# Performance work log

Measured on AMD Instinct MI355X. Metric: run time of the kernel, lower is better.

Reference implementation:

```python
import jax, jax.numpy as jnp
import numpy as np

B, D, N, MH, MV = 4, 1024, 2048, 1024, 1024

def setup_inputs() -> dict:
    key = jax.random.key(0)
    k1, k2, k3, k4, k5 = jax.random.split(key, 5)
    return {
        "x": jax.random.normal(k1, (B, D, N), dtype=jnp.float32),
        "W_Q": jax.random.normal(k2, (MH, D), dtype=jnp.float32),
        "W_K": jax.random.normal(k3, (MH, D), dtype=jnp.float32),
        "W_V": jax.random.normal(k4, (MV, D), dtype=jnp.float32),
        "W_O": jax.random.normal(k5, (D, MV), dtype=jnp.float32),
    }

def reference(x, W_Q, W_K, W_V, W_O):
    # x: [b, d, n] (feature-major). Projections: [b, m, n]
    q = jnp.einsum('hd,bdn->bhn', W_Q, x)
    k = jnp.einsum('hd,bdn->bhn', W_K, x)
    v = jnp.einsum('vd,bdn->bvn', W_V, x)
    # scores[b,i,j] = sum_h k[b,h,i] * q[b,h,j]  -> [b, n, n]; NOTE: no 1/sqrt scale (faithful)
    scores = jnp.einsum('bhi,bhj->bij', k, q)
    scores = jax.nn.softmax(scores, axis=-1)
    # v @ scores -> [b, m_V, n]
    attn = jnp.einsum('bvi,bij->bvj', v, scores)
    # W_O @ attn -> [b, d, n]
    return jnp.einsum('dv,bvj->bdj', W_O, attn)
```

## Files before the change

### kernel.cpp

```cpp
#include <hip/hip_runtime.h>
#include <cstddef>
#include <cstdint>

typedef unsigned short u16;
typedef __attribute__((ext_vector_type(8))) short bf16x8;
typedef __attribute__((ext_vector_type(8))) _Float16 f16x8;
typedef __attribute__((ext_vector_type(4))) float f32x4;
typedef __attribute__((ext_vector_type(16))) float f32x16;

#define GLOBAL_AS __attribute__((address_space(1)))
#define LDS_AS __attribute__((address_space(3)))

__device__ __forceinline__ void async16(const u16* g, u16* l) {
    __builtin_amdgcn_global_load_lds((GLOBAL_AS const uint32_t*)g,
                                     (LDS_AS uint32_t*)l, 16, 0, 0);
}

__device__ __forceinline__ u16 f2bf(float f) {
    uint32_t u = __builtin_bit_cast(uint32_t, f);
    uint32_t r = (u + 0x7FFFu + ((u >> 16) & 1u)) >> 16;
    return (u16)r;
}

__global__ __launch_bounds__(256)
void wcast(const float4* __restrict__ src, u16* __restrict__ dst)
{
    int i = blockIdx.x * 256 + threadIdx.x;
    float4 v = src[i];
    ushort4 a = { f2bf(v.x), f2bf(v.y), f2bf(v.z), f2bf(v.w) };
    *(ushort4*)&dst[4 * (size_t)i] = a;
}

__global__ __launch_bounds__(256)
void tsplit_h2(const float* __restrict__ Sb, size_t sBatch,
               u16* __restrict__ Db, size_t dBatch, size_t plane,
               int R, int C)
{
    const float* S = Sb + blockIdx.z * sBatch;
    u16* D = Db + blockIdx.z * dBatch;
    __shared__ float t[32][33];
    int tx = threadIdx.x & 31, ty = threadIdx.x >> 5;
    int c0 = blockIdx.x * 32, r0 = blockIdx.y * 32;
    #pragma unroll
    for (int k = 0; k < 4; ++k)
        t[ty + 8 * k][tx] = S[(size_t)(r0 + ty + 8 * k) * C + c0 + tx];
    __syncthreads();
    #pragma unroll
    for (int k = 0; k < 4; ++k) {
        float a = t[tx][ty + 8 * k] * 64.0f;
        _Float16 h0 = (_Float16)a;
        _Float16 h1 = (_Float16)(a - (float)h0);
        size_t o = (size_t)(c0 + ty + 8 * k) * R + r0 + tx;
        D[o] = __builtin_bit_cast(u16, h0);
        D[plane + o] = __builtin_bit_cast(u16, h1);
    }
}

__global__ __launch_bounds__(256)
void xprep(const float* __restrict__ Sb, size_t sBatch,
           u16* __restrict__ BFb, size_t bfBatch,
           u16* __restrict__ Db, size_t dBatch, size_t plane)
{
    const float* S = Sb + blockIdx.z * sBatch;
    u16* BF = BFb + blockIdx.z * bfBatch;
    u16* D = Db + blockIdx.z * dBatch;
    __shared__ float t[32][33];
    int tx = threadIdx.x & 31, ty = threadIdx.x >> 5;
    int c0 = blockIdx.x * 32, r0 = blockIdx.y * 32;
    #pragma unroll
    for (int k = 0; k < 4; ++k) {
        float v = S[(size_t)(r0 + ty + 8 * k) * 2048 + c0 + tx];
        t[ty + 8 * k][tx] = v;
        BF[(size_t)(r0 + ty + 8 * k) * 2048 + c0 + tx] = f2bf(v);
    }
    __syncthreads();
    #pragma unroll
    for (int k = 0; k < 4; ++k) {
        float a = t[tx][ty + 8 * k] * 64.0f;
        _Float16 h0 = (_Float16)a;
        _Float16 h1 = (_Float16)(a - (float)h0);
        size_t o = (size_t)(c0 + ty + 8 * k) * 1024 + r0 + tx;
        D[o] = __builtin_bit_cast(u16, h0);
        D[plane + o] = __builtin_bit_cast(u16, h1);
    }
}

__global__ __launch_bounds__(256)
void tcast(const float* __restrict__ S, u16* __restrict__ D, int R, int C)
{
    __shared__ float t[32][33];
    int tx = threadIdx.x & 31, ty = threadIdx.x >> 5;
    int c0 = blockIdx.x * 32, r0 = blockIdx.y * 32;
    #pragma unroll
    for (int k = 0; k < 4; ++k)
        t[ty + 8 * k][tx] = S[(size_t)(r0 + ty + 8 * k) * C + c0 + tx];
    __syncthreads();
    #pragma unroll
    for (int k = 0; k < 4; ++k)
        D[(size_t)(c0 + ty + 8 * k) * R + r0 + tx] = f2bf(t[tx][ty + 8 * k]);
}

__global__ __launch_bounds__(256)
void tbf16(const u16* __restrict__ Sb, size_t sBatch, u16* __restrict__ Db, size_t dBatch)
{
    const u16* S = Sb + blockIdx.z * sBatch;
    u16* D = Db + blockIdx.z * dBatch;
    __shared__ u16 t[32][34];
    int tx = threadIdx.x & 31, ty = threadIdx.x >> 5;
    int c0 = blockIdx.x * 32, r0 = blockIdx.y * 32;
    #pragma unroll
    for (int k = 0; k < 4; ++k)
        t[ty + 8 * k][tx] = S[(size_t)(r0 + ty + 8 * k) * 2048 + c0 + tx];
    __syncthreads();
    #pragma unroll
    for (int k = 0; k < 4; ++k)
        D[(size_t)(c0 + ty + 8 * k) * 2048 + r0 + tx] = t[tx][ty + 8 * k];
}

#define MMF4(AF, BF)                                                                   \
    _Pragma("unroll") for (int i = 0; i < 4; ++i)                                      \
        _Pragma("unroll") for (int j = 0; j < 4; ++j)                                  \
            acc[i][j] = __builtin_amdgcn_mfma_f32_16x16x32_f16(AF[i], BF[j], acc[i][j], 0, 0, 0);
#define MMB4(AF, BF)                                                                   \
    _Pragma("unroll") for (int i = 0; i < 4; ++i)                                      \
        _Pragma("unroll") for (int j = 0; j < 4; ++j)                                  \
            acc[i][j] = __builtin_amdgcn_mfma_f32_16x16x32_bf16(AF[i], BF[j], acc[i][j], 0, 0, 0);

template<int TERMS, int EPI>
__global__ __launch_bounds__(256)
void gemm_big(const u16* __restrict__ Ab, size_t aBatch, size_t aPlane,
              const u16* __restrict__ Bb, size_t bBatch, size_t bPlane,
              void* __restrict__ Cb, size_t cBatch, size_t cPlane,
              int M, int N, int K)
{
    constexpr int RSZ = 4096;
    constexpr int BUF = (TERMS == 3 ? 4 : 2) * RSZ;
    __shared__ u16 lds[2 * BUF];
    const u16* A = Ab + blockIdx.z * aBatch;
    const u16* B = Bb + blockIdx.z * bBatch;
    const int tid = threadIdx.x;
    const int lane = tid & 63, wave = tid >> 6;
    const int m0 = blockIdx.y * 128, n0 = blockIdx.x * 128;
    const int l15 = lane & 15, q = lane >> 4;
    const int rm = (wave >> 1) * 64, rn = (wave & 1) * 64;

    int sr[2], sg[2], sbase[2];
    #pragma unroll
    for (int it = 0; it < 2; ++it) {
        int s = tid + it * 256;
        sr[it] = s >> 2;
        sg[it] = (s & 3) ^ ((sr[it] >> 1) & 3);
        sbase[it] = (it * 256 + wave * 64) * 8;
    }
    const int fsw = (q ^ ((l15 >> 1) & 3)) * 8;
    int aoff[4], boff[4];
    #pragma unroll
    for (int f = 0; f < 4; ++f) {
        aoff[f] = (rm + f * 16 + l15) * 32 + fsw;
        boff[f] = (rn + f * 16 + l15) * 32 + fsw;
    }

    f32x4 acc[4][4];
    #pragma unroll
    for (int i = 0; i < 4; ++i)
        #pragma unroll
        for (int j = 0; j < 4; ++j)
            acc[i][j] = (f32x4){0.f, 0.f, 0.f, 0.f};

#define STAGEB(PP, KT)                                                                 \
    do {                                                                               \
        _Pragma("unroll")                                                              \
        for (int it = 0; it < 2; ++it) {                                               \
            const size_t ao = (size_t)(m0 + sr[it]) * K + (KT) + sg[it] * 8;           \
            const size_t bo = (size_t)(n0 + sr[it]) * K + (KT) + sg[it] * 8;           \
            const int d = (PP) * BUF + sbase[it];                                      \
            if (TERMS == 3) {                                                          \
                async16(A + ao, &lds[d]);                                              \
                async16(A + aPlane + ao, &lds[d + RSZ]);                               \
                async16(B + bo, &lds[d + 2 * RSZ]);                                    \
                async16(B + bPlane + bo, &lds[d + 3 * RSZ]);                           \
            } else {                                                                   \
                async16(A + ao, &lds[d]);                                              \
                async16(B + bo, &lds[d + RSZ]);                                        \
            }                                                                          \
        }                                                                              \
    } while (0)

    STAGEB(0, 0);
    for (int kt = 0; kt < K; kt += 32) {
        const int p = (kt >> 5) & 1;
        __syncthreads();
        if (kt + 32 < K) STAGEB(p ^ 1, kt + 32);
        const u16* L = &lds[p * BUF];
        if (TERMS == 3) {
            f16x8 a0f[4], b0f[4], xf[4];
            #pragma unroll
            for (int f = 0; f < 4; ++f) a0f[f] = *(const f16x8*)&L[aoff[f]];
            #pragma unroll
            for (int f = 0; f < 4; ++f) b0f[f] = *(const f16x8*)&L[2 * RSZ + boff[f]];
            MMF4(a0f, b0f);
            #pragma unroll
            for (int f = 0; f < 4; ++f) xf[f] = *(const f16x8*)&L[3 * RSZ + boff[f]];
            MMF4(a0f, xf);
            #pragma unroll
            for (int f = 0; f < 4; ++f) xf[f] = *(const f16x8*)&L[RSZ + aoff[f]];
            MMF4(xf, b0f);
        } else {
            bf16x8 af[4], bf_[4];
            #pragma unroll
            for (int f = 0; f < 4; ++f) af[f] = *(const bf16x8*)&L[aoff[f]];
            #pragma unroll
            for (int f = 0; f < 4; ++f) bf_[f] = *(const bf16x8*)&L[RSZ + boff[f]];
            MMB4(af, bf_);
        }
    }
#undef STAGEB

    #pragma unroll
    for (int i = 0; i < 4; ++i) {
        int row = m0 + rm + i * 16 + q * 4;
        #pragma unroll
        for (int j = 0; j < 4; ++j) {
            int col = n0 + rn + j * 16 + l15;
            #pragma unroll
            for (int r = 0; r < 4; ++r) {
                float v = acc[i][j][r];
                size_t o = (size_t)(row + r) * N + col;
                if (EPI == 0) {
                    ((float*)Cb + blockIdx.z * cBatch)[o] = v;
                } else if (EPI == 1) {
                    u16* C0 = (u16*)Cb + blockIdx.z * cBatch;
                    float vs = v * 0.000244140625f;
                    _Float16 h0 = (_Float16)vs;
                    _Float16 h1 = (_Float16)(vs - (float)h0);
                    C0[o] = __builtin_bit_cast(u16, h0);
                    C0[cPlane + o] = __builtin_bit_cast(u16, h1);
                } else {
                    ((u16*)Cb + blockIdx.z * cBatch)[o] = f2bf(v);
                }
            }
        }
    }
}

template<int TERMS, int EPI, int TM, int TN, int WGM, int WGN>
__global__ __launch_bounds__(512, 2)
void gemm_w(const u16* __restrict__ Ab, size_t aBatch, size_t aPlane,
            const u16* __restrict__ Bb, size_t bBatch, size_t bPlane,
            void* __restrict__ Cb, size_t cBatch, size_t cPlane,
            int M, int N, int K)
{
    constexpr int ASZ = TM * 32;
    constexpr int BSZ = TN * 32;
    constexpr int APL = (TERMS == 3) ? 2 : 1;
    constexpr int BUF = APL * (ASZ + BSZ);
    constexpr int FM = TM / WGM / 32;
    constexpr int FN = TN / WGN / 32;
    constexpr int AIT = TM / 128;
    constexpr int BIT = TN / 128;
    extern __shared__ __align__(16) u16 lds[];

    int bid = blockIdx.x + gridDim.x * blockIdx.y;
    int cpr = gridDim.x >> 2;
    int c8 = bid & 7, kk = bid >> 3;
    int bx = (kk % cpr) * 4 + (c8 & 3);
    int by = (kk / cpr) * 2 + (c8 >> 2);

    const u16* A = Ab + blockIdx.z * aBatch;
    const u16* B = Bb + blockIdx.z * bBatch;
    const int tid = threadIdx.x;
    const int lane = tid & 63, wave = tid >> 6;
    const int m0 = by * TM, n0 = bx * TN;
    const int l31 = lane & 31, half = lane >> 5;
    const int rm = (wave / WGN) * (TM / WGM);
    const int rn = (wave % WGN) * (TN / WGN);

    int arow[FM], asw[FM], brow[FN], bsw[FN];
    #pragma unroll
    for (int f = 0; f < FM; ++f) { arow[f] = rm + f * 32 + l31; asw[f] = (arow[f] >> 1) & 3; }
    #pragma unroll
    for (int f = 0; f < FN; ++f) { brow[f] = rn + f * 32 + l31; bsw[f] = (brow[f] >> 1) & 3; }

    f32x16 acc[FM][FN];
    #pragma unroll
    for (int i = 0; i < FM; ++i)
        #pragma unroll
        for (int j = 0; j < FN; ++j)
            #pragma unroll
            for (int r = 0; r < 16; ++r) acc[i][j][r] = 0.f;

    auto stage = [&](int pp, int kt) {
        #pragma unroll
        for (int it = 0; it < AIT; ++it) {
            int s = tid + it * 512;
            int r = s >> 2;
            int g = (s & 3) ^ ((r >> 1) & 3);
            int base = pp * BUF + (it * 512 + wave * 64) * 8;
            size_t go = (size_t)(m0 + r) * K + kt + g * 8;
            async16(A + go, &lds[base]);
            if (TERMS == 3) async16(A + aPlane + go, &lds[base + ASZ]);
        }
        #pragma unroll
        for (int it = 0; it < BIT; ++it) {
            int s = tid + it * 512;
            int r = s >> 2;
            int g = (s & 3) ^ ((r >> 1) & 3);
            int base = pp * BUF + APL * ASZ + (it * 512 + wave * 64) * 8;
            size_t go = (size_t)(n0 + r) * K + kt + g * 8;
            async16(B + go, &lds[base]);
            if (TERMS == 3) async16(B + bPlane + go, &lds[base + BSZ]);
        }
    };

#define RDAF(dst, PL, H)                                                               \
    _Pragma("unroll")                                                                  \
    for (int f = 0; f < FM; ++f)                                                       \
        dst[f] = *(const f16x8*)&L[(PL) * ASZ + arow[f] * 32 + ((2 * (H) + half) ^ asw[f]) * 8];
#define RDBF(dst, PL, H)                                                               \
    _Pragma("unroll")                                                                  \
    for (int f = 0; f < FN; ++f)                                                       \
        dst[f] = *(const f16x8*)&L[2 * ASZ + (PL) * BSZ + brow[f] * 32 + ((2 * (H) + half) ^ bsw[f]) * 8];
#define MMW(AF, BF)                                                                    \
    _Pragma("unroll")                                                                  \
    for (int i = 0; i < FM; ++i)                                                       \
        _Pragma("unroll")                                                              \
        for (int j = 0; j < FN; ++j)                                                   \
            acc[i][j] = __builtin_amdgcn_mfma_f32_32x32x16_f16(AF[i], BF[j], acc[i][j], 0, 0, 0);
#define MMWB(AF, BF)                                                                   \
    _Pragma("unroll")                                                                  \
    for (int i = 0; i < FM; ++i)                                                       \
        _Pragma("unroll")                                                              \
        for (int j = 0; j < FN; ++j)                                                   \
            acc[i][j] = __builtin_amdgcn_mfma_f32_32x32x16_bf16(AF[i], BF[j], acc[i][j], 0, 0, 0);

    stage(0, 0);
    for (int kt = 0; kt < K; kt += 32) {
        const int p = (kt >> 5) & 1;
        __syncthreads();
        if (kt + 32 < K) stage(p ^ 1, kt + 32);
        const u16* L = &lds[p * BUF];
        if (TERMS == 3) {
            f16x8 A0h0[FM], A0h1[FM], B0h0[FN], B0h1[FN];
            f16x8 B1h0[FN], B1h1[FN], A1h0[FM], A1h1[FM];
            RDAF(A0h0, 0, 0) RDBF(B0h0, 0, 0)
            RDAF(A0h1, 0, 1) RDBF(B0h1, 0, 1)
            RDBF(B1h0, 1, 0)
            MMW(A0h0, B0h0)
            RDBF(B1h1, 1, 1)
            MMW(A0h1, B0h1)
            RDAF(A1h0, 1, 0)
            MMW(A0h0, B1h0)
            MMW(A0h1, B1h1)
            RDAF(A1h1, 1, 1)
            MMW(A1h0, B0h0)
            MMW(A1h1, B0h1)
        } else {
            bf16x8 Ah0[FM], Ah1[FM], Bh0[FN], Bh1[FN];
            #pragma unroll
            for (int f = 0; f < FM; ++f)
                Ah0[f] = *(const bf16x8*)&L[arow[f] * 32 + (half ^ asw[f]) * 8];
            #pragma unroll
            for (int f = 0; f < FN; ++f)
                Bh0[f] = *(const bf16x8*)&L[ASZ + brow[f] * 32 + (half ^ bsw[f]) * 8];
            #pragma unroll
            for (int f = 0; f < FM; ++f)
                Ah1[f] = *(const bf16x8*)&L[arow[f] * 32 + ((2 + half) ^ asw[f]) * 8];
            #pragma unroll
            for (int f = 0; f < FN; ++f)
                Bh1[f] = *(const bf16x8*)&L[ASZ + brow[f] * 32 + ((2 + half) ^ bsw[f]) * 8];
            MMWB(Ah0, Bh0)
            MMWB(Ah1, Bh1)
        }
    }
#undef RDAF
#undef RDBF
#undef MMW
#undef MMWB

    #pragma unroll
    for (int i = 0; i < FM; ++i) {
        #pragma unroll
        for (int j = 0; j < FN; ++j) {
            int col = n0 + rn + j * 32 + l31;
            #pragma unroll
            for (int r = 0; r < 16; ++r) {
                int row = m0 + rm + i * 32 + (r & 3) + 8 * (r >> 2) + 4 * half;
                float v = acc[i][j][r];
                size_t o = (size_t)row * N + col;
                if (EPI == 0) {
                    ((float*)Cb + blockIdx.z * cBatch)[o] = v;
                } else if (EPI == 1) {
                    u16* C0 = (u16*)Cb + blockIdx.z * cBatch;
                    float vs = v * 0.000244140625f;
                    _Float16 h0 = (_Float16)vs;
                    _Float16 h1 = (_Float16)(vs - (float)h0);
                    C0[o] = __builtin_bit_cast(u16, h0);
                    C0[cPlane + o] = __builtin_bit_cast(u16, h1);
                } else {
                    ((u16*)Cb + blockIdx.z * cBatch)[o] = f2bf(v);
                }
            }
        }
    }
}

__global__ __launch_bounds__(256)
void softmax_p(const float* __restrict__ Sb, size_t sBatch, u16* __restrict__ Pb, size_t pBatch)
{
    const float* S = Sb + blockIdx.y * sBatch + (size_t)blockIdx.x * 2048;
    u16* P = Pb + blockIdx.y * pBatch + (size_t)blockIdx.x * 2048;
    const int tid = threadIdx.x;

    float4 v0 = *(const float4*)&S[tid * 4];
    float4 v1 = *(const float4*)&S[1024 + tid * 4];

    float m = fmaxf(fmaxf(fmaxf(v0.x, v0.y), fmaxf(v0.z, v0.w)),
                    fmaxf(fmaxf(v1.x, v1.y), fmaxf(v1.z, v1.w)));
    #pragma unroll
    for (int off = 32; off > 0; off >>= 1)
        m = fmaxf(m, __shfl_xor(m, off, 64));
    __shared__ float redm[4];
    if ((tid & 63) == 0) redm[tid >> 6] = m;
    __syncthreads();
    m = fmaxf(fmaxf(redm[0], redm[1]), fmaxf(redm[2], redm[3]));

    v0.x = __expf(v0.x - m); v0.y = __expf(v0.y - m);
    v0.z = __expf(v0.z - m); v0.w = __expf(v0.w - m);
    v1.x = __expf(v1.x - m); v1.y = __expf(v1.y - m);
    v1.z = __expf(v1.z - m); v1.w = __expf(v1.w - m);

    float s = v0.x + v0.y + v0.z + v0.w + v1.x + v1.y + v1.z + v1.w;
    #pragma unroll
    for (int off = 32; off > 0; off >>= 1)
        s += __shfl_xor(s, off, 64);
    __shared__ float reds[4];
    if ((tid & 63) == 0) reds[tid >> 6] = s;
    __syncthreads();
    s = reds[0] + reds[1] + reds[2] + reds[3];

    const float r = 1.0f / s;
    ushort4 o0 = { f2bf(v0.x * r), f2bf(v0.y * r), f2bf(v0.z * r), f2bf(v0.w * r) };
    ushort4 o1 = { f2bf(v1.x * r), f2bf(v1.y * r), f2bf(v1.z * r), f2bf(v1.w * r) };
    *(ushort4*)&P[tid * 4] = o0;
    *(ushort4*)&P[1024 + tid * 4] = o1;
}

extern "C" void kernel_launch(void* const* d_in, const int* in_sizes, int n_in,
                              void* d_out, int out_size, void* d_ws, size_t ws_size,
                              hipStream_t stream)
{
    const size_t MB = 1048576;
    const size_t WREG = 34 * MB;
    const size_t PER  = 32 * MB;
    const size_t PER_US = PER / 2, PER_F = PER / 4;

    char* ws = (char*)d_ws;
    u16* WQT2 = (u16*)ws;
    u16* WKT2 = (u16*)(ws + 4 * MB);
    u16* M2   = (u16*)(ws + 8 * MB);
    u16* WObf = (u16*)(ws + 12 * MB);
    u16* WVT  = (u16*)(ws + 14 * MB);
    u16* WOV  = (u16*)(ws + 16 * MB);
    u16* xbf  = (u16*)(ws + 18 * MB);

    int G = (ws_size >= WREG + 4 * PER) ? 4 : (ws_size >= WREG + 2 * PER) ? 2 : 1;

    const float* x = (const float*)d_in[0];
    float* out = (float*)d_out;
    dim3 blk(256);

    hipFuncSetAttribute((const void*)gemm_w<3, 0, 256, 256, 2, 4>,
                        hipFuncAttributeMaxDynamicSharedMemorySize, 131072);
    hipFuncSetAttribute((const void*)gemm_w<3, 1, 256, 128, 4, 2>,
                        hipFuncAttributeMaxDynamicSharedMemorySize, 98304);

    tsplit_h2<<<dim3(32, 32, 1), blk, 0, stream>>>((const float*)d_in[1], 0, WQT2, 0, 1048576, 1024, 1024);
    tsplit_h2<<<dim3(32, 32, 1), blk, 0, stream>>>((const float*)d_in[2], 0, WKT2, 0, 1048576, 1024, 1024);
    gemm_big<3, 1><<<dim3(8, 8, 1), blk, 0, stream>>>(WKT2, 0, 1048576, WQT2, 0, 1048576,
                                                      M2, 0, 1048576, 1024, 1024, 1024);
    wcast<<<1024, blk, 0, stream>>>((const float4*)d_in[4], WObf);
    tcast<<<dim3(32, 32, 1), blk, 0, stream>>>((const float*)d_in[3], WVT, 1024, 1024);
    gemm_big<1, 2><<<dim3(8, 8, 1), blk, 0, stream>>>(WObf, 0, 0, WVT, 0, 0,
                                                      WOV, 0, 0, 1024, 1024, 1024);

    for (int b0 = 0; b0 < 4; b0 += G) {
        char* R = ws + WREG;
        u16*   xT2 = (u16*)R;
        u16*   TT2 = (u16*)(R + 8 * MB);
        float* S32 = (float*)(R + 16 * MB);
        u16*   Pb  = (u16*)R;
        u16*   PTb = (u16*)(R + 8 * MB);
        u16*   XPT = (u16*)(R + 16 * MB);

        xprep<<<dim3(64, 32, G), blk, 0, stream>>>(x + (size_t)b0 * 2097152, 2097152,
                                                   xbf + (size_t)b0 * 2097152, 2097152,
                                                   xT2, PER_US, 2097152);
        gemm_w<3, 1, 256, 128, 4, 2><<<dim3(8, 8, G), 512, 98304, stream>>>(
            xT2, PER_US, 2097152, M2, 0, 1048576, TT2, PER_US, 2097152, 2048, 1024, 1024);
        gemm_w<3, 0, 256, 256, 2, 4><<<dim3(8, 8, G), 512, 131072, stream>>>(
            xT2, PER_US, 2097152, TT2, PER_US, 2097152, S32, PER_F, 0, 2048, 2048, 1024);
        softmax_p<<<dim3(2048, G), blk, 0, stream>>>(S32, PER_F, Pb, PER_US);
        tbf16<<<dim3(64, 64, G), blk, 0, stream>>>(Pb, PER_US, PTb, PER_US);
        gemm_w<1, 2, 256, 128, 4, 2><<<dim3(8, 8, G), 512, 49152, stream>>>(
            PTb, PER_US, 0, xbf + (size_t)b0 * 2097152, 2097152, 0,
            XPT, PER_US, 0, 2048, 1024, 2048);
        gemm_w<1, 0, 256, 128, 4, 2><<<dim3(16, 4, G), 512, 49152, stream>>>(
            WOV, 0, 0, XPT, PER_US, 0, out + (size_t)b0 * 2097152, 2097152, 0,
            1024, 2048, 1024);
    }
}
```

Before: 412.3 us.

## Fuse weight prep kernels and split-K the weight-product GEMMs with reduction

Merges the four weight-conversion kernels into one launch, using a role index in the z grid dimension. The two 1024^3 weight-product GEMMs (W_K^T W_Q and W_O W_V) previously launched only 64 blocks each; they now split K four ways to launch 256 blocks, writing fp32 partials that a new reduce kernel sums and converts. The goal is better occupancy of the many CUs on these small GEMMs and fewer launches. The cost is extra partial-buffer traffic, two added reduce launches, and reuse of the per-batch workspace region for the partials.

```diff
diff --git a/kernel.cpp b/kernel.cpp
--- a/kernel.cpp
+++ b/kernel.cpp
@@ -23,36 +23,44 @@
 }
 
 __global__ __launch_bounds__(256)
-void wcast(const float4* __restrict__ src, u16* __restrict__ dst)
-{
-    int i = blockIdx.x * 256 + threadIdx.x;
-    float4 v = src[i];
-    ushort4 a = { f2bf(v.x), f2bf(v.y), f2bf(v.z), f2bf(v.w) };
-    *(ushort4*)&dst[4 * (size_t)i] = a;
-}
-
-__global__ __launch_bounds__(256)
-void tsplit_h2(const float* __restrict__ Sb, size_t sBatch,
-               u16* __restrict__ Db, size_t dBatch, size_t plane,
-               int R, int C)
-{
-    const float* S = Sb + blockIdx.z * sBatch;
-    u16* D = Db + blockIdx.z * dBatch;
+void wprep(const float* __restrict__ WQ, const float* __restrict__ WK,
+           const float* __restrict__ WV, const float* __restrict__ WO,
+           u16* __restrict__ DQ, u16* __restrict__ DK,
+           u16* __restrict__ DV, u16* __restrict__ DOb)
+{
+    const int role = blockIdx.z;
     __shared__ float t[32][33];
     int tx = threadIdx.x & 31, ty = threadIdx.x >> 5;
     int c0 = blockIdx.x * 32, r0 = blockIdx.y * 32;
+    const float* S = role == 0 ? WQ : role == 1 ? WK : role == 2 ? WV : WO;
+
+    if (role == 3) {
+        #pragma unroll
+        for (int k = 0; k < 4; ++k) {
+            size_t o = (size_t)(r0 + ty + 8 * k) * 1024 + c0 + tx;
+            DOb[o] = f2bf(S[o]);
+        }
+        return;
+    }
     #pragma unroll
     for (int k = 0; k < 4; ++k)
-        t[ty + 8 * k][tx] = S[(size_t)(r0 + ty + 8 * k) * C + c0 + tx];
+        t[ty + 8 * k][tx] = S[(size_t)(r0 + ty + 8 * k) * 1024 + c0 + tx];
     __syncthreads();
-    #pragma unroll
-    for (int k = 0; k < 4; ++k) {
-        float a = t[tx][ty + 8 * k] * 64.0f;
-        _Float16 h0 = (_Float16)a;
-        _Float16 h1 = (_Float16)(a - (float)h0);
-        size_t o = (size_t)(c0 + ty + 8 * k) * R + r0 + tx;
-        D[o] = __builtin_bit_cast(u16, h0);
-        D[plane + o] = __builtin_bit_cast(u16, h1);
+    if (role == 2) {
+        #pragma unroll
+        for (int k = 0; k < 4; ++k)
+            DV[(size_t)(c0 + ty + 8 * k) * 1024 + r0 + tx] = f2bf(t[tx][ty + 8 * k]);
+    } else {
+        u16* D = role == 0 ? DQ : DK;
+        #pragma unroll
+        for (int k = 0; k < 4; ++k) {
+            float a = t[tx][ty + 8 * k] * 64.0f;
+            _Float16 h0 = (_Float16)a;
+            _Float16 h1 = (_Float16)(a - (float)h0);
+            size_t o = (size_t)(c0 + ty + 8 * k) * 1024 + r0 + tx;
+            D[o] = __builtin_bit_cast(u16, h0);
+            D[1048576 + o] = __builtin_bit_cast(u16, h1);
+        }
     }
 }
 
@@ -83,21 +91,6 @@
         D[o] = __builtin_bit_cast(u16, h0);
         D[plane + o] = __builtin_bit_cast(u16, h1);
     }
-}
-
-__global__ __launch_bounds__(256)
-void tcast(const float* __restrict__ S, u16* __restrict__ D, int R, int C)
-{
-    __shared__ float t[32][33];
-    int tx = threadIdx.x & 31, ty = threadIdx.x >> 5;
-    int c0 = blockIdx.x * 32, r0 = blockIdx.y * 32;
-    #pragma unroll
-    for (int k = 0; k < 4; ++k)
-        t[ty + 8 * k][tx] = S[(size_t)(r0 + ty + 8 * k) * C + c0 + tx];
-    __syncthreads();
-    #pragma unroll
-    for (int k = 0; k < 4; ++k)
-        D[(size_t)(c0 + ty + 8 * k) * R + r0 + tx] = f2bf(t[tx][ty + 8 * k]);
 }
 
 __global__ __launch_bounds__(256)
@@ -126,18 +119,21 @@
         _Pragma("unroll") for (int j = 0; j < 4; ++j)                                  \
             acc[i][j] = __builtin_amdgcn_mfma_f32_16x16x32_bf16(AF[i], BF[j], acc[i][j], 0, 0, 0);
 
-template<int TERMS, int EPI>
+template<int TERMS, int SPLITK>
 __global__ __launch_bounds__(256)
-void gemm_big(const u16* __restrict__ Ab, size_t aBatch, size_t aPlane,
-              const u16* __restrict__ Bb, size_t bBatch, size_t bPlane,
-              void* __restrict__ Cb, size_t cBatch, size_t cPlane,
+void gemm_big(const u16* __restrict__ Ab, size_t aPlane,
+              const u16* __restrict__ Bb, size_t bPlane,
+              float* __restrict__ Cb, size_t cBatch,
               int M, int N, int K)
 {
     constexpr int RSZ = 4096;
     constexpr int BUF = (TERMS == 3 ? 4 : 2) * RSZ;
     __shared__ u16 lds[2 * BUF];
-    const u16* A = Ab + blockIdx.z * aBatch;
-    const u16* B = Bb + blockIdx.z * bBatch;
+    const u16* A = Ab;
+    const u16* B = Bb;
+    const int z = blockIdx.z;
+    const int kt0 = SPLITK ? z * (K >> 2) : 0;
+    const int kend = SPLITK ? kt0 + (K >> 2) : K;
     const int tid = threadIdx.x;
     const int lane = tid & 63, wave = tid >> 6;
     const int m0 = blockIdx.y * 128, n0 = blockIdx.x * 128;
@@ -186,11 +182,11 @@
         }                                                                              \
     } while (0)
 
-    STAGEB(0, 0);
-    for (int kt = 0; kt < K; kt += 32) {
+    STAGEB(0, kt0);
+    for (int kt = kt0; kt < kend; kt += 32) {
         const int p = (kt >> 5) & 1;
         __syncthreads();
-        if (kt + 32 < K) STAGEB(p ^ 1, kt + 32);
+        if (kt + 32 < kend) STAGEB(p ^ 1, kt + 32);
         const u16* L = &lds[p * BUF];
         if (TERMS == 3) {
             f16x8 a0f[4], b0f[4], xf[4];
@@ -216,6 +212,7 @@
     }
 #undef STAGEB
 
+    float* C = Cb + (size_t)z * cBatch;
     #pragma unroll
     for (int i = 0; i < 4; ++i) {
         int row = m0 + rm + i * 16 + q * 4;
@@ -223,94 +220,34 @@
         for (int j = 0; j < 4; ++j) {
             int col = n0 + rn + j * 16 + l15;
             #pragma unroll
-            for (int r = 0; r < 4; ++r) {
-                float v = acc[i][j][r];
-                size_t o = (size_t)(row + r) * N + col;
-                if (EPI == 0) {
-                    ((float*)Cb + blockIdx.z * cBatch)[o] = v;
-                } else if (EPI == 1) {
-                    u16* C0 = (u16*)Cb + blockIdx.z * cBatch;
-                    float vs = v * 0.000244140625f;
-                    _Float16 h0 = (_Float16)vs;
-                    _Float16 h1 = (_Float16)(vs - (float)h0);
-                    C0[o] = __builtin_bit_cast(u16, h0);
-                    C0[cPlane + o] = __builtin_bit_cast(u16, h1);
-                } else {
-                    ((u16*)Cb + blockIdx.z * cBatch)[o] = f2bf(v);
-                }
-            }
-        }
-    }
-}
-
-template<int TERMS, int EPI, int TM, int TN, int WGM, int WGN>
-__global__ __launch_bounds__(512, 2)
-void gemm_w(const u16* __restrict__ Ab, size_t aBatch, size_t aPlane,
-            const u16* __restrict__ Bb, size_t bBatch, size_t bPlane,
-            void* __restrict__ Cb, size_t cBatch, size_t cPlane,
-            int M, int N, int K)
-{
-    constexpr int ASZ = TM * 32;
-    constexpr int BSZ = TN * 32;
-    constexpr int APL = (TERMS == 3) ? 2 : 1;
-    constexpr int BUF = APL * (ASZ + BSZ);
-    constexpr int FM = TM / WGM / 32;
-    constexpr int FN = TN / WGN / 32;
-    constexpr int AIT = TM / 128;
-    constexpr int BIT = TN / 128;
-    extern __shared__ __align__(16) u16 lds[];
-
-    int bid = blockIdx.x + gridDim.x * blockIdx.y;
-    int cpr = gridDim.x >> 2;
-    int c8 = bid & 7, kk = bid >> 3;
-    int bx = (kk % cpr) * 4 + (c8 & 3);
-    int by = (kk / cpr) * 2 + (c8 >> 2);
-
-    const u16* A = Ab + blockIdx.z * aBatch;
-    const u16* B = Bb + blockIdx.z * bBatch;
-    const int tid = threadIdx.x;
-    const int lane = tid & 63, wave = tid >> 6;
-    const int m0 = by * TM, n0 = bx * TN;
-    const int l31 = lane & 31, half = lane >> 5;
-    const int rm = (wave / WGN) * (TM / WGM);
-    const int rn = (wave % WGN) * (TN / WGN);
-
-    int arow[FM], asw[FM], brow[FN], bsw[FN];
-    #pragma unroll
-    for (int f = 0; f < FM; ++f) { arow[f] = rm + f * 32 + l31; asw[f] = (arow[f] >> 1) & 3; }
-    #pragma unroll
-    for (int f = 0; f < FN; ++f) { brow[f] = rn + f * 32 + l31; bsw[f] = (brow[f] >> 1) & 3; }
-
-    f32x16 acc[FM][FN];
-    #pragma unroll
-    for (int i = 0; i < FM; ++i)
-        #pragma unroll
-        for (int j = 0; j < FN; ++j)
-            #pragma unroll
-            for (int r = 0; r < 16; ++r) acc[i][j][r] = 0.f;
-
-    auto stage = [&](int pp, int kt) {
-        #pragma unroll
-        for (int it = 0; it < AIT; ++it) {
-            int s = tid + it * 512;
-            int r = s >> 2;
-            int g = (s & 3) ^ ((r >> 1) & 3);
-            int base = pp * BUF + (it * 512 + wave * 64) * 8;
-            size_t go = (size_t)(m0 + r) * K + kt + g * 8;
-            async16(A + go, &lds[base]);
-            if (TERMS == 3) async16(A + aPlane + go, &lds[base + ASZ]);
-        }
-        #pragma unroll
-        for (int it = 0; it < BIT; ++it) {
-            int s = tid + it * 512;
-            int r = s >> 2;
-            int g = (s & 3) ^ ((r >> 1) & 3);
-            int base = pp * BUF + APL * ASZ + (it * 512 + wave * 64) * 8;
-            size_t go = (size_t)(n0 + r) * K + kt + g * 8;
-            async16(B + go, &lds[base]);
-            if (TERMS == 3) async16(B + bPlane + go, &lds[base + BSZ]);
-        }
-    };
+            for (int r = 0; r < 4; ++r)
+                C[(size_t)(row + r) * N + col] = acc[i][j][r];
+        }
+    }
+}
+
+template<int EPI>
+__global__ __launch_bounds__(256)
+void reduce4(const float4* __restrict__ P, u16* __restrict__ D, size_t plane)
+{
+    size_t i = blockIdx.x * 256 + threadIdx.x;
+    float4 a = P[i], b = P[262144 + i], c = P[524288 + i], d = P[786432 + i];
+    float v[4] = { a.x + b.x + c.x + d.x, a.y + b.y + c.y + d.y,
+                   a.z + b.z + c.z + d.z, a.w + b.w + c.w + d.w };
+    if (EPI == 1) {
+        #pragma unroll
+        for (int k = 0; k < 4; ++k) {
+            float vs = v[k] * 0.000244140625f;
+            _Float16 h0 = (_Float16)vs;
+            _Float16 h1 = (_Float16)(vs - (float)h0);
+            D[i * 4 + k] = __builtin_bit_cast(u16, h0);
+            D[plane + i * 4 + k] = __builtin_bit_cast(u16, h1);
+        }
+    } else {
+        ushort4 o = { f2bf(v[0]), f2bf(v[1]), f2bf(v[2]), f2bf(v[3]) };
+        *(ushort4*)&D[i * 4] = o;
+    }
+}
 
 #define RDAF(dst, PL, H)                                                               \
     _Pragma("unroll")                                                                  \
@@ -332,6 +269,75 @@
         _Pragma("unroll")                                                              \
         for (int j = 0; j < FN; ++j)                                                   \
             acc[i][j] = __builtin_amdgcn_mfma_f32_32x32x16_bf16(AF[i], BF[j], acc[i][j], 0, 0, 0);
+
+template<int TERMS, int EPI, int TM, int TN, int WGM, int WGN>
+__global__ __launch_bounds__(512, 2)
+void gemm_w(const u16* __restrict__ Ab, size_t aBatch, size_t aPlane,
+            const u16* __restrict__ Bb, size_t bBatch, size_t bPlane,
+            void* __restrict__ Cb, size_t cBatch, size_t cPlane,
+            int M, int N, int K)
+{
+    constexpr int ASZ = TM * 32;
+    constexpr int BSZ = TN * 32;
+    constexpr int APL = (TERMS == 3) ? 2 : 1;
+    constexpr int BUF = APL * (ASZ + BSZ);
+    constexpr int FM = TM / WGM / 32;
+    constexpr int FN = TN / WGN / 32;
+    constexpr int AIT = TM / 128;
+    constexpr int BIT = TN / 128;
+    extern __shared__ __align__(16) u16 lds[];
+
+    int bid = blockIdx.x + gridDim.x * blockIdx.y;
+    int cpr = gridDim.x >> 2;
+    int c8 = bid & 7, kk = bid >> 3;
+    int bx = (kk % cpr) * 4 + (c8 & 3);
+    int by = (kk / cpr) * 2 + (c8 >> 2);
+
+    const u16* A = Ab + blockIdx.z * aBatch;
+    const u16* B = Bb + blockIdx.z * bBatch;
+    const int tid = threadIdx.x;
+    const int lane = tid & 63, wave = tid >> 6;
+    const int m0 = by * TM, n0 = bx * TN;
+    const int l31 = lane & 31, half = lane >> 5;
+    const int rm = (wave / WGN) * (TM / WGM);
+    const int rn = (wave % WGN) * (TN / WGN);
+
+    int arow[FM], asw[FM], brow[FN], bsw[FN];
+    #pragma unroll
+    for (int f = 0; f < FM; ++f) { arow[f] = rm + f * 32 + l31; asw[f] = (arow[f] >> 1) & 3; }
+    #pragma unroll
+    for (int f = 0; f < FN; ++f) { brow[f] = rn + f * 32 + l31; bsw[f] = (brow[f] >> 1) & 3; }
+
+    f32x16 acc[FM][FN];
+    #pragma unroll
+    for (int i = 0; i < FM; ++i)
+        #pragma unroll
+        for (int j = 0; j < FN; ++j)
+            #pragma unroll
+            for (int r = 0; r < 16; ++r) acc[i][j][r] = 0.f;
+
+    auto stage = [&](int pp, int kt) {
+        #pragma unroll
+        for (int it = 0; it < AIT; ++it) {
+            int s = tid + it * 512;
+            int r = s >> 2;
+            int g = (s & 3) ^ ((r >> 1) & 3);
+            int base = pp * BUF + (it * 512 + wave * 64) * 8;
+            size_t go = (size_t)(m0 + r) * K + kt + g * 8;
+            async16(A + go, &lds[base]);
+            if (TERMS == 3) async16(A + aPlane + go, &lds[base + ASZ]);
+        }
+        #pragma unroll
+        for (int it = 0; it < BIT; ++it) {
+            int s = tid + it * 512;
+            int r = s >> 2;
+            int g = (s & 3) ^ ((r >> 1) & 3);
+            int base = pp * BUF + APL * ASZ + (it * 512 + wave * 64) * 8;
+            size_t go = (size_t)(n0 + r) * K + kt + g * 8;
+            async16(B + go, &lds[base]);
+            if (TERMS == 3) async16(B + bPlane + go, &lds[base + BSZ]);
+        }
+    };
 
     stage(0, 0);
     for (int kt = 0; kt < K; kt += 32) {
@@ -372,10 +378,6 @@
             MMWB(Ah1, Bh1)
         }
     }
-#undef RDAF
-#undef RDBF
-#undef MMW
-#undef MMWB
 
     #pragma unroll
     for (int i = 0; i < FM; ++i) {
@@ -404,6 +406,11 @@
     }
 }
 
+#undef RDAF
+#undef RDBF
+#undef MMW
+#undef MMWB
+
 __global__ __launch_bounds__(256)
 void softmax_p(const float* __restrict__ Sb, size_t sBatch, u16* __restrict__ Pb, size_t pBatch)
 {
@@ -474,14 +481,17 @@
     hipFuncSetAttribute((const void*)gemm_w<3, 1, 256, 128, 4, 2>,
                         hipFuncAttributeMaxDynamicSharedMemorySize, 98304);
 
-    tsplit_h2<<<dim3(32, 32, 1), blk, 0, stream>>>((const float*)d_in[1], 0, WQT2, 0, 1048576, 1024, 1024);
-    tsplit_h2<<<dim3(32, 32, 1), blk, 0, stream>>>((const float*)d_in[2], 0, WKT2, 0, 1048576, 1024, 1024);
-    gemm_big<3, 1><<<dim3(8, 8, 1), blk, 0, stream>>>(WKT2, 0, 1048576, WQT2, 0, 1048576,
-                                                      M2, 0, 1048576, 1024, 1024, 1024);
-    wcast<<<1024, blk, 0, stream>>>((const float4*)d_in[4], WObf);
-    tcast<<<dim3(32, 32, 1), blk, 0, stream>>>((const float*)d_in[3], WVT, 1024, 1024);
-    gemm_big<1, 2><<<dim3(8, 8, 1), blk, 0, stream>>>(WObf, 0, 0, WVT, 0, 0,
-                                                      WOV, 0, 0, 1024, 1024, 1024);
+    float* PART = (float*)(ws + WREG);
+    wprep<<<dim3(32, 32, 4), blk, 0, stream>>>(
+        (const float*)d_in[1], (const float*)d_in[2],
+        (const float*)d_in[3], (const float*)d_in[4],
+        WQT2, WKT2, WVT, WObf);
+    gemm_big<3, 1><<<dim3(8, 8, 4), blk, 0, stream>>>(WKT2, 1048576, WQT2, 1048576,
+                                                      PART, 1048576, 1024, 1024, 1024);
+    reduce4<1><<<1024, blk, 0, stream>>>((const float4*)PART, M2, 1048576);
+    gemm_big<1, 1><<<dim3(8, 8, 4), blk, 0, stream>>>(WObf, 0, WVT, 0,
+                                                      PART, 1048576, 1024, 1024, 1024);
+    reduce4<2><<<1024, blk, 0, stream>>>((const float4*)PART, WOV, 0);
 
     for (int b0 = 0; b0 < 4; b0 += G) {
         char* R = ws + WREG;
```

Result: faster. 393.5 us (-4.6%).
